# Optimization experiments

Hardware: AMD Instinct MI355X
Metric: run time of the kernel (lower is better)

## Reference

```python
import jax, jax.numpy as jnp
import numpy as np

D_HIDDEN = 1024
NUM_HEADS = 16
D_HEAD = D_HIDDEN // NUM_HEADS


def setup_inputs() -> dict:
    key = jax.random.key(0)
    ks = jax.random.split(key, 9)
    N, S, D = 4, 2048, D_HIDDEN
    s = 1.0 / np.sqrt(D)
    inp = {
        "x": jax.random.normal(ks[0], (N, S, D), dtype=jnp.float32),
        "Wq": jax.random.uniform(ks[1], (D, D), jnp.float32, -s, s),
        "bq": jnp.zeros((D,), jnp.float32),
        "Wk": jax.random.uniform(ks[2], (D, D), jnp.float32, -s, s),
        "bk": jnp.zeros((D,), jnp.float32),
        "Wv": jax.random.uniform(ks[3], (D, D), jnp.float32, -s, s),
        "bv": jnp.zeros((D,), jnp.float32),
        "Wo": jax.random.uniform(ks[4], (D, D), jnp.float32, -s, s),
        "bo": jnp.zeros((D,), jnp.float32),
        "ln_gamma": jnp.ones((D,), jnp.float32),
        "ln_beta": jnp.zeros((D,), jnp.float32),
    }
    return inp


def _layer_norm(x, gamma, beta, eps=1e-5):
    mu = jnp.mean(x, axis=-1, keepdims=True)
    var = jnp.var(x, axis=-1, keepdims=True)
    return (x - mu) * jax.lax.rsqrt(var + eps) * gamma + beta


def reference(x, Wq, bq, Wk, bk, Wv, bv, Wo, bo, ln_gamma, ln_beta):
    N, S, D = x.shape
    H, Dh = NUM_HEADS, D_HEAD
    xn = _layer_norm(x, ln_gamma, ln_beta)
    # torch Linear: y = x @ W.T + b
    q = (xn @ Wq.T + bq).reshape(N, S, H, Dh)
    k = (xn @ Wk.T + bk).reshape(N, S, H, Dh)
    v = (xn @ Wv.T + bv).reshape(N, S, H, Dh)
    # scores: [N, H, S, S]
    scores = jnp.einsum('nxhd,nyhd->nhxy', q, k) / np.sqrt(Dh)
    # causal mask: positions y > x get -inf
    mask = jnp.triu(jnp.full((S, S), -jnp.inf, dtype=scores.dtype), k=1)
    attn = jax.nn.softmax(scores + mask[None, None], axis=-1)
    z = jnp.einsum('nhxy,nyhd->nxhd', attn, v).reshape(N, S, D)
    return z @ Wo.T + bo
```

## Files before the change

### kernel.cpp

```cpp
#include <hip/hip_runtime.h>

typedef unsigned short u16;
typedef unsigned int   u32;
typedef __bf16 bf16x8 __attribute__((ext_vector_type(8)));
typedef float  f32x4  __attribute__((ext_vector_type(4)));
typedef unsigned short u16x8 __attribute__((ext_vector_type(8)));
typedef unsigned short u16x4 __attribute__((ext_vector_type(4)));

#define SEQ 2048
#define DM  1024
#define TOKS 8388608
#define SCLQ 0.18033688f

__device__ __forceinline__ float bf2f(u16 u) {
    u32 i = ((u32)u) << 16;
    float f; __builtin_memcpy(&f, &i, 4); return f;
}
__device__ __forceinline__ u16 f2bf(float f) {
    u32 i; __builtin_memcpy(&i, &f, 4);
    return (u16)((i + 0x7FFFu + ((i >> 16) & 1u)) >> 16);
}
__device__ __forceinline__ bf16x8 ld8(const u16* p) {
    return __builtin_bit_cast(bf16x8, *(const u16x8*)p);
}
#define GLD16(src, dst) __builtin_amdgcn_global_load_lds( \
    (const __attribute__((address_space(1))) void*)(src), \
    (__attribute__((address_space(3))) void*)(dst), 16, 0, 0)

#define SBAR() do { asm volatile("" ::: "memory"); __builtin_amdgcn_sched_barrier(0); \
    __builtin_amdgcn_s_barrier(); __builtin_amdgcn_sched_barrier(0); asm volatile("" ::: "memory"); } while (0)
#define WVM(n) asm volatile("s_waitcnt vmcnt(" #n ")" ::: "memory")

__global__ __launch_bounds__(64) void detect_k(const u32* __restrict__ x, int* __restrict__ flag) {
    const int lane = threadIdx.x;
    u32 w = x[lane];
    int e0 = (int)((w >> 7) & 0xFFu);
    int cnt = (e0 >= 100 && e0 <= 140) ? 1 : 0;
#pragma unroll
    for (int off = 32; off; off >>= 1) cnt += __shfl_xor(cnt, off);
    if (lane == 0) *flag = (cnt < 32) ? 1 : 0;
}

__global__ __launch_bounds__(256) void convert_k(const void* s0, const void* s1, const void* s2, const void* s3,
                                                 const void* v0, const void* v1, const void* v2, const void* v3,
                                                 const void* v4, const void* v5,
                                                 u16* __restrict__ dstW, u16* __restrict__ dstV,
                                                 const int* __restrict__ flagp) {
    const int y = blockIdx.y, tid = threadIdx.x;
    const int fp32m = *flagp;
    const void* src; u16* dst; size_t off;
    if (y < 4) {
        src = (y == 0) ? s0 : (y == 1) ? s1 : (y == 2) ? s2 : s3;
        dst = dstW + (size_t)y * 1048576;
        off = (size_t)blockIdx.x * 1024 + tid * 4;
    } else {
        const int i = blockIdx.x;
        if (i >= 6) return;
        src = (i == 0) ? v0 : (i == 1) ? v1 : (i == 2) ? v2 : (i == 3) ? v3 : (i == 4) ? v4 : v5;
        dst = dstV + (size_t)i * 1024;
        off = (size_t)tid * 4;
    }
    u16x4 o;
    if (fp32m) {
        const float* f = (const float*)src + off;
#pragma unroll
        for (int j = 0; j < 4; ++j) o[j] = f2bf(f[j]);
    } else {
        o = *(const u16x4*)((const u16*)src + off);
    }
    *(u16x4*)(dst + off) = o;
}

__global__ __launch_bounds__(256) void ln_k(const void* __restrict__ xv,
                                            const u16* __restrict__ g,
                                            const u16* __restrict__ b,
                                            u16* __restrict__ xn,
                                            const int* __restrict__ flagp) {
    const int row = blockIdx.x, tid = threadIdx.x;
    const int fp32m = *flagp;
    float f[4], s1 = 0.f, s2 = 0.f;
    if (fp32m) {
        f32x4 v = *(const f32x4*)((const float*)xv + (size_t)row * DM + tid * 4);
#pragma unroll
        for (int j = 0; j < 4; ++j) f[j] = v[j];
    } else {
        u16x4 v = *(const u16x4*)((const u16*)xv + (size_t)row * DM + tid * 4);
#pragma unroll
        for (int j = 0; j < 4; ++j) f[j] = bf2f(v[j]);
    }
#pragma unroll
    for (int j = 0; j < 4; ++j) { s1 += f[j]; s2 += f[j] * f[j]; }
#pragma unroll
    for (int off = 32; off; off >>= 1) { s1 += __shfl_xor(s1, off); s2 += __shfl_xor(s2, off); }
    __shared__ float red[8];
    const int wave = tid >> 6, lane = tid & 63;
    if (lane == 0) { red[wave] = s1; red[4 + wave] = s2; }
    __syncthreads();
    s1 = red[0] + red[1] + red[2] + red[3];
    s2 = red[4] + red[5] + red[6] + red[7];
    const float mu = s1 * (1.f / DM);
    const float var = s2 * (1.f / DM) - mu * mu;
    const float rs = rsqrtf(var + 1e-5f);
    u16x4 gv = *(const u16x4*)(g + tid * 4);
    u16x4 bv = *(const u16x4*)(b + tid * 4);
    u16x4 o;
#pragma unroll
    for (int j = 0; j < 4; ++j) o[j] = f2bf((f[j] - mu) * rs * bf2f(gv[j]) + bf2f(bv[j]));
    *(u16x4*)(xn + (size_t)row * DM + tid * 4) = o;
}

__global__ __launch_bounds__(512, 2) void gemm_qkv_k(const u16* __restrict__ xn, const u16* __restrict__ Wc,
                                                     const u16* __restrict__ Vc,
                                                     u16* __restrict__ Q, u16* __restrict__ K, u16* __restrict__ Vt) {
    __shared__ alignas(16) u16 lds[65536];
    const int tid = threadIdx.x;
    const int w = tid >> 6, lane = tid & 63;
    const int l4 = lane & 15, q4 = lane >> 4;
    const int bm = blockIdx.x, bn = blockIdx.y;
    const int wm0 = (w >> 2) * 128, wn = (w & 3) * 64;

    const int srow = lane >> 3, schk = (lane & 7) ^ srow;
    const u16* aS = xn + ((size_t)(bm * 256) + srow) * DM + schk * 8;
    const u16* bS = Wc + ((size_t)(bn * 256) + srow) * DM + schk * 8;
    const int bg0 = (w >> 1) * 64 + (w & 1) * 16;

    auto STG = [&](int h, int kt, int bufb) {
        const size_t kk = (size_t)kt * 64;
        u16* ld0 = lds + bufb * 32768;
        if (h == 0) {
            GLD16(aS + (size_t)(8 * w) * DM + kk,        ld0 + (8 * w) * 64);
            GLD16(aS + (size_t)(128 + 8 * w) * DM + kk,  ld0 + (128 + 8 * w) * 64);
        } else if (h == 2) {
            GLD16(aS + (size_t)(64 + 8 * w) * DM + kk,   ld0 + (64 + 8 * w) * 64);
            GLD16(aS + (size_t)(192 + 8 * w) * DM + kk,  ld0 + (192 + 8 * w) * 64);
        } else {
            const int b0 = bg0 + ((h == 3) ? 32 : 0);
            GLD16(bS + (size_t)b0 * DM + kk,             ld0 + 16384 + b0 * 64);
            GLD16(bS + (size_t)(b0 + 8) * DM + kk,       ld0 + 16384 + (b0 + 8) * 64);
        }
    };

    const int swz0 = (q4 ^ (l4 & 7)) << 3;
    const int swz1 = ((4 + q4) ^ (l4 & 7)) << 3;
    const int arow = (wm0 + l4) * 64;
    const int brow = 16384 + (wn + l4) * 64;

    f32x4 acc[8][4] = {};
    bf16x8 afLo[4][2], afHi[4][2], bfr[2][2];

    STG(0, 0, 0); STG(1, 0, 0); STG(2, 0, 0); STG(3, 0, 0);

#pragma unroll
    for (int kt = 0; kt < 16; ++kt) {
        const int buf = kt & 1, nxt = buf ^ 1;
        const u16* bp = lds + buf * 32768;
        const bool pf = (kt < 15);
        WVM(4); SBAR();
        if (pf) STG(0, kt + 1, nxt);
#pragma unroll
        for (int mt = 0; mt < 4; ++mt) {
            afLo[mt][0] = ld8(bp + arow + mt * 1024 + swz0);
            afLo[mt][1] = ld8(bp + arow + mt * 1024 + swz1);
        }
#pragma unroll
        for (int nt = 0; nt < 2; ++nt) {
            bfr[nt][0] = ld8(bp + brow + nt * 1024 + swz0);
            bfr[nt][1] = ld8(bp + brow + nt * 1024 + swz1);
        }
        __builtin_amdgcn_s_setprio(1);
#pragma unroll
        for (int mt = 0; mt < 4; ++mt)
#pragma unroll
            for (int nt = 0; nt < 2; ++nt) {
                acc[mt][nt] = __builtin_amdgcn_mfma_f32_16x16x32_bf16(afLo[mt][0], bfr[nt][0], acc[mt][nt], 0, 0, 0);
                acc[mt][nt] = __builtin_amdgcn_mfma_f32_16x16x32_bf16(afLo[mt][1], bfr[nt][1], acc[mt][nt], 0, 0, 0);
            }
        __builtin_amdgcn_s_setprio(0);
        if (pf) { WVM(4); } else { WVM(2); }
        SBAR();
        if (pf) STG(1, kt + 1, nxt);
#pragma unroll
        for (int mt = 0; mt < 4; ++mt) {
            afHi[mt][0] = ld8(bp + arow + (mt + 4) * 1024 + swz0);
            afHi[mt][1] = ld8(bp + arow + (mt + 4) * 1024 + swz1);
        }
        __builtin_amdgcn_s_setprio(1);
#pragma unroll
        for (int mt = 0; mt < 4; ++mt)
#pragma unroll
            for (int nt = 0; nt < 2; ++nt) {
                acc[mt + 4][nt] = __builtin_amdgcn_mfma_f32_16x16x32_bf16(afHi[mt][0], bfr[nt][0], acc[mt + 4][nt], 0, 0, 0);
                acc[mt + 4][nt] = __builtin_amdgcn_mfma_f32_16x16x32_bf16(afHi[mt][1], bfr[nt][1], acc[mt + 4][nt], 0, 0, 0);
            }
        __builtin_amdgcn_s_setprio(0);
        if (pf) { WVM(4); } else { WVM(0); }
        SBAR();
        if (pf) STG(2, kt + 1, nxt);
#pragma unroll
        for (int nt = 0; nt < 2; ++nt) {
            bfr[nt][0] = ld8(bp + brow + (nt + 2) * 1024 + swz0);
            bfr[nt][1] = ld8(bp + brow + (nt + 2) * 1024 + swz1);
        }
        __builtin_amdgcn_s_setprio(1);
#pragma unroll
        for (int mt = 0; mt < 4; ++mt)
#pragma unroll
            for (int nt = 0; nt < 2; ++nt) {
                acc[mt + 4][nt + 2] = __builtin_amdgcn_mfma_f32_16x16x32_bf16(afHi[mt][0], bfr[nt][0], acc[mt + 4][nt + 2], 0, 0, 0);
                acc[mt + 4][nt + 2] = __builtin_amdgcn_mfma_f32_16x16x32_bf16(afHi[mt][1], bfr[nt][1], acc[mt + 4][nt + 2], 0, 0, 0);
            }
        __builtin_amdgcn_s_setprio(0);
        SBAR();
        if (pf) STG(3, kt + 1, nxt);
        __builtin_amdgcn_s_setprio(1);
#pragma unroll
        for (int mt = 0; mt < 4; ++mt)
#pragma unroll
            for (int nt = 0; nt < 2; ++nt) {
                acc[mt][nt + 2] = __builtin_amdgcn_mfma_f32_16x16x32_bf16(afLo[mt][0], bfr[nt][0], acc[mt][nt + 2], 0, 0, 0);
                acc[mt][nt + 2] = __builtin_amdgcn_mfma_f32_16x16x32_bf16(afLo[mt][1], bfr[nt][1], acc[mt][nt + 2], 0, 0, 0);
            }
        __builtin_amdgcn_s_setprio(0);
    }

    const int whichB = bn >> 2;
    const int cb = (bn & 3) * 256 + wn;
    u16* outp = (whichB == 0) ? Q : (whichB == 1) ? K : Vt;
    const float scl = (whichB == 0) ? SCLQ : 1.0f;
#pragma unroll
    for (int nt = 0; nt < 4; ++nt) {
        const int cc = cb + nt * 16 + l4;
        const float bs = bf2f(Vc[whichB * 1024 + cc]);
#pragma unroll
        for (int mt = 0; mt < 8; ++mt) {
            const int row0 = bm * 256 + wm0 + mt * 16 + q4 * 4;
            if (whichB < 2) {
#pragma unroll
                for (int r = 0; r < 4; ++r)
                    outp[(size_t)(row0 + r) * DM + cc] = f2bf((acc[mt][nt][r] + bs) * scl);
            } else {
                const int nb = row0 >> 11, s0 = row0 & 2047;
                u16x4 pk;
#pragma unroll
                for (int r = 0; r < 4; ++r) pk[r] = f2bf(acc[mt][nt][r] + bs);
                *(u16x4*)(outp + ((size_t)(nb * 1024 + cc)) * SEQ + s0) = pk;
            }
        }
    }
}

#define LDS_U16 73728

__device__ __forceinline__ void wait_vm12() { asm volatile("s_waitcnt vmcnt(12)" ::: "memory"); }
__device__ __forceinline__ void wait_vm6()  { asm volatile("s_waitcnt vmcnt(6)"  ::: "memory"); }
__device__ __forceinline__ void wait_vm0()  { asm volatile("s_waitcnt vmcnt(0)"  ::: "memory"); }

__device__ __forceinline__ void gemm256x128_out(u16* lds,
                                                const u16* __restrict__ A,
                                                const u16* __restrict__ W,
                                                const u16* __restrict__ bias,
                                                u16* __restrict__ o0,
                                                int fp32m) {
    const int tid = threadIdx.x;
    const int w = tid >> 6, lane = tid & 63;
    const int l4 = lane & 15, q4 = lane >> 4;
    const int bm = blockIdx.x, bn = blockIdx.y;
    const int wm = (w >> 1) * 64, wn = (w & 1) * 64;

    const int srow = lane >> 3;
    const int schk = (lane & 7) ^ srow;
    const u16* sA = A + ((size_t)(bm * 256 + w * 32 + srow)) * DM + (schk << 3);
    const u16* sB = W + ((size_t)(bn * 128 + w * 16 + srow)) * DM + (schk << 3);

    int offA[4][2], offB[4][2];
#pragma unroll
    for (int mt = 0; mt < 4; ++mt)
#pragma unroll
        for (int s = 0; s < 2; ++s) {
            const int row = wm + mt * 16 + l4;
            offA[mt][s] = row * 64 + (((s * 4 + q4) ^ (l4 & 7)) << 3);
        }
#pragma unroll
    for (int nt = 0; nt < 4; ++nt)
#pragma unroll
        for (int s = 0; s < 2; ++s) {
            const int row = wn + nt * 16 + l4;
            offB[nt][s] = 16384 + row * 64 + (((s * 4 + q4) ^ (l4 & 7)) << 3);
        }

    auto STAGE = [&](int kt, int b) {
        const u16* a0 = sA + kt * 64;
        const u16* b0 = sB + kt * 64;
        u16* la = lds + b * 24576 + w * 2048;
        u16* lb = lds + b * 24576 + 16384 + w * 1024;
        GLD16(a0,           la);
        GLD16(a0 + 8 * DM,  la + 512);
        GLD16(a0 + 16 * DM, la + 1024);
        GLD16(a0 + 24 * DM, la + 1536);
        GLD16(b0,           lb);
        GLD16(b0 + 8 * DM,  lb + 512);
    };

    f32x4 acc[4][4] = {};

    STAGE(0, 0); STAGE(1, 1); STAGE(2, 2);

#pragma unroll
    for (int kt = 0; kt < 16; ++kt) {
        const int b = kt % 3;
        if (kt < 14)      wait_vm12();
        else if (kt == 14) wait_vm6();
        else               wait_vm0();
        __builtin_amdgcn_s_barrier();
        __builtin_amdgcn_sched_barrier(0);
        const u16* base = lds + b * 24576;
        bf16x8 af[4][2], bfr[4][2];
#pragma unroll
        for (int mt = 0; mt < 4; ++mt)
#pragma unroll
            for (int s = 0; s < 2; ++s) af[mt][s] = ld8(base + offA[mt][s]);
#pragma unroll
        for (int nt = 0; nt < 2; ++nt)
#pragma unroll
            for (int s = 0; s < 2; ++s) bfr[nt][s] = ld8(base + offB[nt][s]);
        __builtin_amdgcn_s_setprio(1);
#pragma unroll
        for (int mt = 0; mt < 4; ++mt)
#pragma unroll
            for (int nt = 0; nt < 2; ++nt)
#pragma unroll
                for (int s = 0; s < 2; ++s)
                    acc[mt][nt] = __builtin_amdgcn_mfma_f32_16x16x32_bf16(af[mt][s], bfr[nt][s], acc[mt][nt], 0, 0, 0);
        __builtin_amdgcn_s_setprio(0);
#pragma unroll
        for (int nt = 2; nt < 4; ++nt)
#pragma unroll
            for (int s = 0; s < 2; ++s) bfr[nt][s] = ld8(base + offB[nt][s]);
        __builtin_amdgcn_s_setprio(1);
#pragma unroll
        for (int mt = 0; mt < 4; ++mt)
#pragma unroll
            for (int nt = 2; nt < 4; ++nt)
#pragma unroll
                for (int s = 0; s < 2; ++s)
                    acc[mt][nt] = __builtin_amdgcn_mfma_f32_16x16x32_bf16(af[mt][s], bfr[nt][s], acc[mt][nt], 0, 0, 0);
        __builtin_amdgcn_s_setprio(0);
        __builtin_amdgcn_s_barrier();
        __builtin_amdgcn_sched_barrier(0);
        if (kt < 13) STAGE(kt + 3, b);
    }

#pragma unroll
    for (int nt = 0; nt < 4; ++nt) {
        const int cc = bn * 128 + wn + nt * 16 + l4;
        const float bs = bf2f(bias[cc]);
#pragma unroll
        for (int mt = 0; mt < 4; ++mt) {
            const int row0 = bm * 256 + wm + mt * 16 + q4 * 4;
            if (fp32m) {
#pragma unroll
                for (int r = 0; r < 4; ++r)
                    ((float*)o0)[(size_t)(row0 + r) * DM + cc] = acc[mt][nt][r] + bs;
            } else {
#pragma unroll
                for (int r = 0; r < 4; ++r)
                    o0[(size_t)(row0 + r) * DM + cc] = f2bf(acc[mt][nt][r] + bs);
            }
        }
    }
}

__global__ __launch_bounds__(512, 2) void gemm_out_k(const u16* __restrict__ Z, const u16* __restrict__ Wc,
                                                     const u16* __restrict__ Vc,
                                                     u16* __restrict__ out, const int* __restrict__ flagp) {
    __shared__ alignas(16) u16 lds[LDS_U16];
    const int fp32m = *flagp;
    gemm256x128_out(lds, Z, Wc + 3 * 1048576, Vc + 3 * 1024, out, fp32m);
}

__global__ __launch_bounds__(256, 4) void flash_k(const u16* __restrict__ Q,
                                                  const u16* __restrict__ K,
                                                  const u16* __restrict__ Vt,
                                                  u16* __restrict__ Z) {
    const int bh = blockIdx.x;
    const int qb = 15 - (int)blockIdx.y;
    const int n = bh >> 4, h = bh & 15;
    const int tid = threadIdx.x, wave = tid >> 6, lane = tid & 63;
    const int l4 = lane & 15, q4 = lane >> 4;

    __shared__ alignas(16) u16 Ks[2][64 * 32];
    __shared__ alignas(16) u16 Vs[2][64 * 32];
    __shared__ alignas(16) u16 Pl[4][2][16 * 72];

    const int Q0w = qb * 128 + wave * 32;
    bf16x8 qf[2][2];
#pragma unroll
    for (int qt = 0; qt < 2; ++qt) {
        const u16* Qr = Q + ((size_t)(n * SEQ + Q0w + qt * 16 + l4)) * DM + h * 64 + q4 * 8;
        qf[qt][0] = ld8(Qr);
        qf[qt][1] = ld8(Qr + 32);
    }

    const int srow = lane >> 2, scol = (lane & 3) * 8;
    const u16* Kg = K + ((size_t)(n * SEQ + wave * 16 + srow)) * DM + h * 64 + scol;
    const u16* Vg = Vt + ((size_t)(n * 1024 + h * 64 + wave * 16 + srow)) * SEQ + scol;
    u16* KsD0 = &Ks[0][wave * 512];
    u16* KsD1 = &Ks[1][wave * 512];
    u16* VsD0 = &Vs[0][wave * 512];
    u16* VsD1 = &Vs[1][wave * 512];

    f32x4 o[2][4] = {};
    float l_acc[2] = {0.f, 0.f};
    const int nch = 2 * qb + 2;

    for (int c = 0; c < nch; ++c) {
        const int kv0 = c * 64;
        const size_t krow = (size_t)kv0 * DM;
        GLD16(Kg + krow, KsD0);
        GLD16(Kg + krow + 32, KsD1);
        GLD16(Vg + kv0, VsD0);
        GLD16(Vg + kv0 + 32, VsD1);
        __syncthreads();

        bf16x8 a[4][2];
#pragma unroll
        for (int mt = 0; mt < 4; ++mt) {
            a[mt][0] = ld8(&Ks[0][(mt * 16 + l4) * 32 + q4 * 8]);
            a[mt][1] = ld8(&Ks[1][(mt * 16 + l4) * 32 + q4 * 8]);
        }
#pragma unroll
        for (int qt = 0; qt < 2; ++qt) {
            f32x4 st[4];
#pragma unroll
            for (int mt = 0; mt < 4; ++mt) {
                f32x4 zz = {0.f, 0.f, 0.f, 0.f};
                st[mt] = __builtin_amdgcn_mfma_f32_16x16x32_bf16(a[mt][0], qf[qt][0], zz, 0, 0, 0);
                st[mt] = __builtin_amdgcn_mfma_f32_16x16x32_bf16(a[mt][1], qf[qt][1], st[mt], 0, 0, 0);
            }
            const int qg = Q0w + qt * 16 + l4;
            u16* P = Pl[wave][qt];
            float la = l_acc[qt];
#pragma unroll
            for (int mt = 0; mt < 4; ++mt) {
                __bf16 pk[4];
#pragma unroll
                for (int r = 0; r < 4; ++r) {
                    const int kv = kv0 + mt * 16 + q4 * 4 + r;
                    float p = __builtin_amdgcn_exp2f(st[mt][r]);
                    p = (kv > qg) ? 0.f : p;
                    la += p;
                    pk[r] = (__bf16)p;
                }
                *(u16x4*)(P + l4 * 72 + mt * 16 + q4 * 4) = *(u16x4*)pk;
            }
            l_acc[qt] = la;
        }
#pragma unroll
        for (int ks = 0; ks < 2; ++ks) {
            bf16x8 pf0 = ld8(&Pl[wave][0][l4 * 72 + ks * 32 + q4 * 8]);
            bf16x8 pf1 = ld8(&Pl[wave][1][l4 * 72 + ks * 32 + q4 * 8]);
#pragma unroll
            for (int nt = 0; nt < 4; ++nt) {
                bf16x8 vf = ld8(&Vs[ks][(nt * 16 + l4) * 32 + q4 * 8]);
                o[0][nt] = __builtin_amdgcn_mfma_f32_16x16x32_bf16(pf0, vf, o[0][nt], 0, 0, 0);
                o[1][nt] = __builtin_amdgcn_mfma_f32_16x16x32_bf16(pf1, vf, o[1][nt], 0, 0, 0);
            }
        }
        __syncthreads();
    }

#pragma unroll
    for (int qt = 0; qt < 2; ++qt) {
        float l = l_acc[qt];
        l += __shfl_xor(l, 16);
        l += __shfl_xor(l, 32);
        float lr[4];
#pragma unroll
        for (int r = 0; r < 4; ++r) lr[r] = 1.f / __shfl(l, q4 * 4 + r);
#pragma unroll
        for (int nt = 0; nt < 4; ++nt) {
            const int col = h * 64 + nt * 16 + l4;
#pragma unroll
            for (int r = 0; r < 4; ++r) {
                const int row = n * SEQ + Q0w + qt * 16 + q4 * 4 + r;
                Z[(size_t)row * DM + col] = f2bf(o[qt][nt][r] * lr[r]);
            }
        }
    }
}

extern "C" void kernel_launch(void* const* d_in, const int* in_sizes, int n_in,
                              void* d_out, int out_size, void* d_ws, size_t ws_size,
                              hipStream_t stream) {
    const void* x  = d_in[0];
    const void* Wq = d_in[1];
    const void* bq = d_in[2];
    const void* Wk = d_in[3];
    const void* bk = d_in[4];
    const void* Wv = d_in[5];
    const void* bv = d_in[6];
    const void* Wo = d_in[7];
    const void* bo = d_in[8];
    const void* g  = d_in[9];
    const void* b  = d_in[10];
    u16* ws = (u16*)d_ws;

    u16* xn  = ws;
    u16* Qb  = ws + (size_t)TOKS;
    u16* Kb  = ws + (size_t)2 * TOKS;
    u16* Vtb = ws + (size_t)3 * TOKS;
    u16* Zb  = ws;
    u16* Wc  = ws + (size_t)4 * TOKS;
    u16* Vc  = Wc + 4 * 1048576;
    int* flagp = (int*)(Vc + 8 * 1024);

    detect_k<<<dim3(1), 64, 0, stream>>>((const u32*)x, flagp);
    convert_k<<<dim3(1024, 5), 256, 0, stream>>>(Wq, Wk, Wv, Wo, bq, bk, bv, bo, g, b, Wc, Vc, flagp);
    ln_k<<<dim3(4 * SEQ), 256, 0, stream>>>(x, Vc + 4 * 1024, Vc + 5 * 1024, xn, flagp);
    gemm_qkv_k<<<dim3(32, 12), 512, 0, stream>>>(xn, Wc, Vc, Qb, Kb, Vtb);
    flash_k<<<dim3(64, 16), 256, 0, stream>>>(Qb, Kb, Vtb, Zb);
    gemm_out_k<<<dim3(32, 8), 512, 0, stream>>>(Zb, Wc, Vc, (u16*)d_out, flagp);
}
```

Measured before the change: 259.0 us.

## Reorder GEMM quadrant schedule to keep one A fragment set live

Reorders the four MFMA quadrants inside each k-step so that only one set of A fragments is held in registers at a time, instead of separate low and high sets. The low B fragments are now re-read from LDS for the last quadrant. The staging order of the next tile's global-to-LDS loads changes to match, and one workgroup barrier per k-step is dropped. The aim is to cut VGPR pressure, which could allow higher occupancy or less spilling. The cost is extra LDS reads and tighter sync reasoning, since the wait counts were left unchanged while the load order moved.

```diff
diff --git a/kernel.cpp b/kernel.cpp
--- a/kernel.cpp
+++ b/kernel.cpp
@@ -146,9 +146,9 @@
     const int brow = 16384 + (wn + l4) * 64;
 
     f32x4 acc[8][4] = {};
-    bf16x8 afLo[4][2], afHi[4][2], bfr[2][2];
-
-    STG(0, 0, 0); STG(1, 0, 0); STG(2, 0, 0); STG(3, 0, 0);
+    bf16x8 afA[4][2], bfr[2][2];
+
+    STG(0, 0, 0); STG(1, 0, 0); STG(3, 0, 0); STG(2, 0, 0);
 
 #pragma unroll
     for (int kt = 0; kt < 16; ++kt) {
@@ -159,8 +159,8 @@
         if (pf) STG(0, kt + 1, nxt);
 #pragma unroll
         for (int mt = 0; mt < 4; ++mt) {
-            afLo[mt][0] = ld8(bp + arow + mt * 1024 + swz0);
-            afLo[mt][1] = ld8(bp + arow + mt * 1024 + swz1);
+            afA[mt][0] = ld8(bp + arow + mt * 1024 + swz0);
+            afA[mt][1] = ld8(bp + arow + mt * 1024 + swz1);
         }
 #pragma unroll
         for (int nt = 0; nt < 2; ++nt) {
@@ -172,53 +172,57 @@
         for (int mt = 0; mt < 4; ++mt)
 #pragma unroll
             for (int nt = 0; nt < 2; ++nt) {
-                acc[mt][nt] = __builtin_amdgcn_mfma_f32_16x16x32_bf16(afLo[mt][0], bfr[nt][0], acc[mt][nt], 0, 0, 0);
-                acc[mt][nt] = __builtin_amdgcn_mfma_f32_16x16x32_bf16(afLo[mt][1], bfr[nt][1], acc[mt][nt], 0, 0, 0);
+                acc[mt][nt] = __builtin_amdgcn_mfma_f32_16x16x32_bf16(afA[mt][0], bfr[nt][0], acc[mt][nt], 0, 0, 0);
+                acc[mt][nt] = __builtin_amdgcn_mfma_f32_16x16x32_bf16(afA[mt][1], bfr[nt][1], acc[mt][nt], 0, 0, 0);
             }
         __builtin_amdgcn_s_setprio(0);
         if (pf) { WVM(4); } else { WVM(2); }
         SBAR();
         if (pf) STG(1, kt + 1, nxt);
 #pragma unroll
-        for (int mt = 0; mt < 4; ++mt) {
-            afHi[mt][0] = ld8(bp + arow + (mt + 4) * 1024 + swz0);
-            afHi[mt][1] = ld8(bp + arow + (mt + 4) * 1024 + swz1);
+        for (int nt = 0; nt < 2; ++nt) {
+            bfr[nt][0] = ld8(bp + brow + (nt + 2) * 1024 + swz0);
+            bfr[nt][1] = ld8(bp + brow + (nt + 2) * 1024 + swz1);
         }
         __builtin_amdgcn_s_setprio(1);
 #pragma unroll
         for (int mt = 0; mt < 4; ++mt)
 #pragma unroll
             for (int nt = 0; nt < 2; ++nt) {
-                acc[mt + 4][nt] = __builtin_amdgcn_mfma_f32_16x16x32_bf16(afHi[mt][0], bfr[nt][0], acc[mt + 4][nt], 0, 0, 0);
-                acc[mt + 4][nt] = __builtin_amdgcn_mfma_f32_16x16x32_bf16(afHi[mt][1], bfr[nt][1], acc[mt + 4][nt], 0, 0, 0);
+                acc[mt][nt + 2] = __builtin_amdgcn_mfma_f32_16x16x32_bf16(afA[mt][0], bfr[nt][0], acc[mt][nt + 2], 0, 0, 0);
+                acc[mt][nt + 2] = __builtin_amdgcn_mfma_f32_16x16x32_bf16(afA[mt][1], bfr[nt][1], acc[mt][nt + 2], 0, 0, 0);
             }
         __builtin_amdgcn_s_setprio(0);
         if (pf) { WVM(4); } else { WVM(0); }
         SBAR();
+        if (pf) STG(3, kt + 1, nxt);
+#pragma unroll
+        for (int mt = 0; mt < 4; ++mt) {
+            afA[mt][0] = ld8(bp + arow + (mt + 4) * 1024 + swz0);
+            afA[mt][1] = ld8(bp + arow + (mt + 4) * 1024 + swz1);
+        }
+        __builtin_amdgcn_s_setprio(1);
+#pragma unroll
+        for (int mt = 0; mt < 4; ++mt)
+#pragma unroll
+            for (int nt = 0; nt < 2; ++nt) {
+                acc[mt + 4][nt + 2] = __builtin_amdgcn_mfma_f32_16x16x32_bf16(afA[mt][0], bfr[nt][0], acc[mt + 4][nt + 2], 0, 0, 0);
+                acc[mt + 4][nt + 2] = __builtin_amdgcn_mfma_f32_16x16x32_bf16(afA[mt][1], bfr[nt][1], acc[mt + 4][nt + 2], 0, 0, 0);
+            }
+        __builtin_amdgcn_s_setprio(0);
         if (pf) STG(2, kt + 1, nxt);
 #pragma unroll
         for (int nt = 0; nt < 2; ++nt) {
-            bfr[nt][0] = ld8(bp + brow + (nt + 2) * 1024 + swz0);
-            bfr[nt][1] = ld8(bp + brow + (nt + 2) * 1024 + swz1);
+            bfr[nt][0] = ld8(bp + brow + nt * 1024 + swz0);
+            bfr[nt][1] = ld8(bp + brow + nt * 1024 + swz1);
         }
         __builtin_amdgcn_s_setprio(1);
 #pragma unroll
         for (int mt = 0; mt < 4; ++mt)
 #pragma unroll
             for (int nt = 0; nt < 2; ++nt) {
-                acc[mt + 4][nt + 2] = __builtin_amdgcn_mfma_f32_16x16x32_bf16(afHi[mt][0], bfr[nt][0], acc[mt + 4][nt + 2], 0, 0, 0);
-                acc[mt + 4][nt + 2] = __builtin_amdgcn_mfma_f32_16x16x32_bf16(afHi[mt][1], bfr[nt][1], acc[mt + 4][nt + 2], 0, 0, 0);
-            }
-        __builtin_amdgcn_s_setprio(0);
-        SBAR();
-        if (pf) STG(3, kt + 1, nxt);
-        __builtin_amdgcn_s_setprio(1);
-#pragma unroll
-        for (int mt = 0; mt < 4; ++mt)
-#pragma unroll
-            for (int nt = 0; nt < 2; ++nt) {
-                acc[mt][nt + 2] = __builtin_amdgcn_mfma_f32_16x16x32_bf16(afLo[mt][0], bfr[nt][0], acc[mt][nt + 2], 0, 0, 0);
-                acc[mt][nt + 2] = __builtin_amdgcn_mfma_f32_16x16x32_bf16(afLo[mt][1], bfr[nt][1], acc[mt][nt + 2], 0, 0, 0);
+                acc[mt + 4][nt] = __builtin_amdgcn_mfma_f32_16x16x32_bf16(afA[mt][0], bfr[nt][0], acc[mt + 4][nt], 0, 0, 0);
+                acc[mt + 4][nt] = __builtin_amdgcn_mfma_f32_16x16x32_bf16(afA[mt][1], bfr[nt][1], acc[mt + 4][nt], 0, 0, 0);
             }
         __builtin_amdgcn_s_setprio(0);
     }
```

Result: no change. 256.1 us (-1.1%).
